# Optimization experiments

Measured on AMD Instinct MI355X. Metric: run time of the kernel, lower is better.

The kernel has to match this reference:

```python
import jax, jax.numpy as jnp
import numpy as np

B, T, EMB = 2, 2048, 1024
H, D = 16, 64          # n_heads, head_dim; H*D == EMB
FF = 4 * EMB


def _ln(x, w, b, eps=1e-5):
    mu = jnp.mean(x, axis=-1, keepdims=True)
    var = jnp.var(x, axis=-1, keepdims=True)
    return (x - mu) * jax.lax.rsqrt(var + eps) * w + b


def setup_inputs() -> dict:
    key = jax.random.key(0)
    ks = jax.random.split(key, 5)
    s = 0.02
    return {
        "x": jax.random.normal(ks[0], (B, T, EMB), jnp.float32),
        "ln1_w": jnp.ones((EMB,), jnp.float32),
        "ln1_b": jnp.zeros((EMB,), jnp.float32),
        "c_proj_w": jax.random.normal(ks[1], (3 * H * D, EMB), jnp.float32) * s,  # Linear(emb, 3HD, bias=False)
        "proj_w": jax.random.normal(ks[2], (EMB, H * D), jnp.float32) * s,
        "proj_b": jnp.zeros((EMB,), jnp.float32),
        "ln2_w": jnp.ones((EMB,), jnp.float32),
        "ln2_b": jnp.zeros((EMB,), jnp.float32),
        "ffn1_w": jax.random.normal(ks[3], (FF, EMB), jnp.float32) * s,
        "ffn1_b": jnp.zeros((FF,), jnp.float32),
        "ffn2_w": jax.random.normal(ks[4], (EMB, FF), jnp.float32) * s,
        "ffn2_b": jnp.zeros((EMB,), jnp.float32),
    }


def reference(x, ln1_w, ln1_b, c_proj_w, proj_w, proj_b, ln2_w, ln2_b,
              ffn1_w, ffn1_b, ffn2_w, ffn2_b):
    Bx, Tx, C = x.shape
    ln_x = _ln(x, ln1_w, ln1_b)
    c = ln_x @ c_proj_w.T                     # (B,T,3HD)
    c = c.reshape(Bx, Tx, H, 3 * D)
    k, q, v = jnp.split(c, 3, axis=-1)        # split order k,q,v as in source
    q = q.transpose(0, 2, 1, 3)               # (B,H,T,D)
    k = k.transpose(0, 2, 1, 3)
    v = v.transpose(0, 2, 1, 3)
    wei = jnp.einsum('bhqd,bhkd->bhqk', q, k) * (D ** -0.5)  # (B,H,T,T)
    mask = jnp.tril(jnp.ones((Tx, Tx), bool))
    wei = jnp.where(mask, wei, -jnp.inf)
    wei = jax.nn.softmax(wei, axis=-1)
    act = jnp.einsum('bhqk,bhkd->bhqd', wei, v)
    act = act.transpose(0, 2, 1, 3).reshape(Bx, Tx, H * D)
    act = act @ proj_w.T + proj_b
    act = x + act                              # residual 1
    h = _ln(act, ln2_w, ln2_b)
    h = jax.nn.relu(h @ ffn1_w.T + ffn1_b) @ ffn2_w.T + ffn2_b
    return x + h                               # NOTE: source adds x, not act
```

## Files before the change

kernel.cpp:

```cpp
#include <hip/hip_runtime.h>
#include <math.h>

typedef unsigned short u16;
typedef unsigned int u32;
typedef __attribute__((ext_vector_type(8))) __bf16 bf16x8;
typedef __attribute__((ext_vector_type(4))) float f32x4;

#define DEVI __device__ __forceinline__

DEVI u16 f2bf(float f){
  u32 b = __builtin_bit_cast(u32, f);
  return (u16)((b + 0x7FFFu + ((b >> 16) & 1u)) >> 16);
}

DEVI f32x4 mfma16(bf16x8 a, bf16x8 b, f32x4 c){
  return __builtin_amdgcn_mfma_f32_16x16x32_bf16(a, b, c, 0, 0, 0);
}

DEVI void gload16(const u16* g, u16* l){
  __builtin_amdgcn_global_load_lds(
      (const __attribute__((address_space(1))) u32*)g,
      (__attribute__((address_space(3))) u32*)l,
      16, 0, 0);
}

DEVI void phase_bar(){
  __builtin_amdgcn_sched_barrier(0);
  __builtin_amdgcn_s_barrier();
  __builtin_amdgcn_sched_barrier(0);
}

__global__ __launch_bounds__(256) void cvt_kernel(const float* __restrict__ in,
                                                  u16* __restrict__ out, int n4){
  int i = blockIdx.x * 256 + threadIdx.x;
  if (i >= n4) return;
  float4 v = reinterpret_cast<const float4*>(in)[i];
  u32 lo = (u32)f2bf(v.x) | ((u32)f2bf(v.y) << 16);
  u32 hi = (u32)f2bf(v.z) | ((u32)f2bf(v.w) << 16);
  reinterpret_cast<uint2*>(out)[i] = make_uint2(lo, hi);
}

__global__ __launch_bounds__(256) void ln_kernel(const float* __restrict__ x,
                                                 const float* __restrict__ w,
                                                 const float* __restrict__ b,
                                                 u16* __restrict__ out){
  int row = blockIdx.x;
  int tid = threadIdx.x;
  const float4 v = reinterpret_cast<const float4*>(x + (size_t)row * 1024)[tid];
  float s  = v.x + v.y + v.z + v.w;
  float ss = v.x*v.x + v.y*v.y + v.z*v.z + v.w*v.w;
  #pragma unroll
  for (int m = 1; m < 64; m <<= 1){
    s  += __shfl_xor(s,  m, 64);
    ss += __shfl_xor(ss, m, 64);
  }
  __shared__ float red[8];
  int wid = tid >> 6, lane = tid & 63;
  if (lane == 0){ red[wid] = s; red[4 + wid] = ss; }
  __syncthreads();
  s  = red[0] + red[1] + red[2] + red[3];
  ss = red[4] + red[5] + red[6] + red[7];
  float mu   = s * (1.0f/1024.0f);
  float var  = ss * (1.0f/1024.0f) - mu*mu;
  float rstd = rsqrtf(var + 1e-5f);
  const float4 wv = reinterpret_cast<const float4*>(w)[tid];
  const float4 bv = reinterpret_cast<const float4*>(b)[tid];
  u32 lo = (u32)f2bf((v.x-mu)*rstd*wv.x + bv.x) | ((u32)f2bf((v.y-mu)*rstd*wv.y + bv.y) << 16);
  u32 hi = (u32)f2bf((v.z-mu)*rstd*wv.z + bv.z) | ((u32)f2bf((v.w-mu)*rstd*wv.w + bv.w) << 16);
  reinterpret_cast<uint2*>(out + (size_t)row*1024)[tid] = make_uint2(lo, hi);
}

__global__ __launch_bounds__(256) void reduce4_kernel(const u16* __restrict__ P,
                                                      const float* __restrict__ x,
                                                      const float* __restrict__ bias,
                                                      float* __restrict__ out){
  const size_t i8 = ((size_t)blockIdx.x * 256 + threadIdx.x) * 8;
  const size_t PS = (size_t)4096 * 1024;
  const int col0 = (int)(i8 & 1023);
  float acc[8];
  #pragma unroll
  for (int j = 0; j < 8; ++j) acc[j] = bias[col0 + j];
  #pragma unroll
  for (int s = 0; s < 4; ++s){
    uint4 d = *reinterpret_cast<const uint4*>(P + s*PS + i8);
    u32 w[4] = {d.x, d.y, d.z, d.w};
    #pragma unroll
    for (int j = 0; j < 8; ++j){
      u32 bits = ((w[j>>1] >> (16*(j&1))) & 0xFFFFu) << 16;
      acc[j] += __builtin_bit_cast(float, bits);
    }
  }
  float4 xv0 = reinterpret_cast<const float4*>(x + i8)[0];
  float4 xv1 = reinterpret_cast<const float4*>(x + i8)[1];
  acc[0]+=xv0.x; acc[1]+=xv0.y; acc[2]+=xv0.z; acc[3]+=xv0.w;
  acc[4]+=xv1.x; acc[5]+=xv1.y; acc[6]+=xv1.z; acc[7]+=xv1.w;
  reinterpret_cast<float4*>(out + i8)[0] = make_float4(acc[0],acc[1],acc[2],acc[3]);
  reinterpret_cast<float4*>(out + i8)[1] = make_float4(acc[4],acc[5],acc[6],acc[7]);
}

template<bool HAS_BIAS, bool RELU, bool SPLIT>
__global__ __launch_bounds__(512, 2) void gemm256(const u16* __restrict__ A,
                                                  const u16* __restrict__ W,
                                                  const float* __restrict__ bias,
                                                  u16* __restrict__ outp,
                                                  int M, int N, int lda, int kLen){
  const int tid = threadIdx.x;
  const int wid = tid >> 6, lane = tid & 63;
  const int l16 = lane & 15, lhi = lane >> 4;
  const int wr = wid >> 2, wc = wid & 3;

  const int gx = gridDim.x, gy = gridDim.y;
  const int nwg = gx * gy * gridDim.z;
  const int bid = (blockIdx.z * gy + blockIdx.y) * gx + blockIdx.x;
  const int swz = (bid & 7) * (nwg >> 3) + (bid >> 3);
  const int col = swz % gx;
  const int rs  = swz / gx;
  const int row = rs % gy;
  const int ksp = rs / gy;
  const int brow = row * 256;
  const int bcol = col * 256;
  const size_t koff = (size_t)ksp * kLen;
  if (SPLIT) outp += (size_t)ksp * M * N;

  __shared__ u16 LDS[2][2][2][256*32];

  const int srow = tid >> 2;
  const int cg   = (tid & 3) ^ ((tid >> 3) & 3);
  const u16* gA = A + (size_t)(brow + srow) * lda + koff + cg*8;
  const u16* gW = W + (size_t)(bcol + srow) * lda + koff + cg*8;
  const size_t rK = (size_t)128 * lda;

#define STAGE(buf, mat, ks, t) do {                                   \
    const u16* _s = ((mat) ? gW : gA) + (t)*64 + (ks)*32;             \
    u16* _d = &LDS[buf][mat][ks][(wid*16)*32];                        \
    gload16(_s,      _d);                                             \
    gload16(_s + rK, _d + 128*32);                                    \
  } while(0)

  const int cswz = (lhi ^ ((l16 >> 1) & 3)) * 8;
  const int aoff = (wr*128 + l16)*32 + cswz;
  const int boff = (wc*64  + l16)*32 + cswz;
#define RDA(buf, ks, m) (*reinterpret_cast<const bf16x8*>(&LDS[buf][0][ks][aoff + (m)*512]))
#define RDB(buf, ks, n) (*reinterpret_cast<const bf16x8*>(&LDS[buf][1][ks][boff + (n)*512]))

  f32x4 acc[8][4] = {};
  bf16x8 a[8], b0, b1;

#define MFMA_PH(n0, n1) do {                                          \
    __builtin_amdgcn_s_setprio(1);                                    \
    _Pragma("unroll")                                                 \
    for (int m = 0; m < 8; ++m){                                      \
      acc[m][n0] = mfma16(a[m], b0, acc[m][n0]);                      \
      acc[m][n1] = mfma16(a[m], b1, acc[m][n1]);                      \
    }                                                                 \
    __builtin_amdgcn_s_setprio(0);                                    \
  } while(0)

  const int NITER = kLen >> 7;

  STAGE(0,0,0,0); STAGE(0,1,0,0); STAGE(0,0,1,0); STAGE(0,1,1,0);
  STAGE(1,0,0,1); STAGE(1,1,0,1);
  asm volatile("s_waitcnt vmcnt(4)" ::: "memory");
  phase_bar();

  for (int j = 0; j < NITER; ++j){
    const int t0 = 2*j, t1 = 2*j + 1;
    const bool more = (j + 1 < NITER);

    #pragma unroll
    for (int m = 0; m < 8; ++m) a[m] = RDA(0,0,m);
    b0 = RDB(0,0,0); b1 = RDB(0,0,1);
    STAGE(1,0,1,t1);
    phase_bar();
    MFMA_PH(0,1);
    phase_bar();
    b0 = RDB(0,0,2); b1 = RDB(0,0,3);
    STAGE(1,1,1,t1);
    phase_bar();
    MFMA_PH(2,3);
    phase_bar();
    #pragma unroll
    for (int m = 0; m < 8; ++m) a[m] = RDA(0,1,m);
    b0 = RDB(0,1,0); b1 = RDB(0,1,1);
    if (more) STAGE(0,0,0,t0+2);
    phase_bar();
    MFMA_PH(0,1);
    phase_bar();
    b0 = RDB(0,1,2); b1 = RDB(0,1,3);
    if (more){ STAGE(0,1,0,t0+2); asm volatile("s_waitcnt vmcnt(4)" ::: "memory"); }
    else     {                    asm volatile("s_waitcnt vmcnt(0)" ::: "memory"); }
    phase_bar();
    MFMA_PH(2,3);
    phase_bar();
    #pragma unroll
    for (int m = 0; m < 8; ++m) a[m] = RDA(1,0,m);
    b0 = RDB(1,0,0); b1 = RDB(1,0,1);
    if (more) STAGE(0,0,1,t0+2);
    phase_bar();
    MFMA_PH(0,1);
    phase_bar();
    b0 = RDB(1,0,2); b1 = RDB(1,0,3);
    if (more) STAGE(0,1,1,t0+2);
    phase_bar();
    MFMA_PH(2,3);
    phase_bar();
    #pragma unroll
    for (int m = 0; m < 8; ++m) a[m] = RDA(1,1,m);
    b0 = RDB(1,1,0); b1 = RDB(1,1,1);
    if (more) STAGE(1,0,0,t1+2);
    phase_bar();
    MFMA_PH(0,1);
    phase_bar();
    b0 = RDB(1,1,2); b1 = RDB(1,1,3);
    if (more){ STAGE(1,1,0,t1+2); asm volatile("s_waitcnt vmcnt(4)" ::: "memory"); }
    phase_bar();
    MFMA_PH(2,3);
    phase_bar();
  }
  __builtin_amdgcn_sched_barrier(0);

  const int row0 = brow + wr*128;
  const int col0 = bcol + wc*64;
  #pragma unroll
  for (int m = 0; m < 8; ++m){
    #pragma unroll
    for (int n = 0; n < 4; ++n){
      #pragma unroll
      for (int r = 0; r < 4; ++r){
        int row_ = row0 + m*16 + 4*lhi + r;
        int col_ = col0 + n*16 + l16;
        float v = acc[m][n][r];
        if constexpr (HAS_BIAS) v += bias[col_];
        if constexpr (RELU)     v = fmaxf(v, 0.0f);
        outp[(size_t)row_ * N + col_] = f2bf(v);
      }
    }
  }
#undef STAGE
#undef RDA
#undef RDB
#undef MFMA_PH
}

template<bool HAS_BIAS, bool HAS_RES, bool RELU, bool OUT_BF16>
__global__ __launch_bounds__(256) void gemm_bt(const u16* __restrict__ A,
                                               const u16* __restrict__ W,
                                               const float* __restrict__ bias,
                                               const float* __restrict__ res,
                                               void* __restrict__ outp,
                                               int M, int N, int K){
  const int tid = threadIdx.x;
  const int wid = tid >> 6, lane = tid & 63;
  const int l16 = lane & 15, lhi = lane >> 4;
  const int wr = wid >> 1, wc = wid & 1;

  const int gx = gridDim.x;
  const int nwg = gx * gridDim.y;
  const int bid = blockIdx.y * gx + blockIdx.x;
  const int swz = (bid & 7) * (nwg >> 3) + (bid >> 3);
  const int brow = (swz / gx) * 128;
  const int bcol = (swz % gx) * 128;

  __shared__ u16 As[2][128*32];
  __shared__ u16 Bs[2][128*32];

  const int srow = wid*32 + (lane >> 2);
  const int schk = lane & 3;
  const u16* gA0 = A + (size_t)(brow + srow)      * K + schk*8;
  const u16* gA1 = A + (size_t)(brow + srow + 16) * K + schk*8;
  const u16* gW0 = W + (size_t)(bcol + srow)      * K + schk*8;
  const u16* gW1 = W + (size_t)(bcol + srow + 16) * K + schk*8;
  const int ldsA0 = (wid*32)*32, ldsA1 = (wid*32 + 16)*32;

  f32x4 acc[4][4] = {};

  gload16(gA0, &As[0][ldsA0]);
  gload16(gA1, &As[0][ldsA1]);
  gload16(gW0, &Bs[0][ldsA0]);
  gload16(gW1, &Bs[0][ldsA1]);

  int cur = 0;
  for (int k0 = 0; k0 < K; k0 += 32){
    __syncthreads();
    if (k0 + 32 < K){
      gload16(gA0 + k0 + 32, &As[cur^1][ldsA0]);
      gload16(gA1 + k0 + 32, &As[cur^1][ldsA1]);
      gload16(gW0 + k0 + 32, &Bs[cur^1][ldsA0]);
      gload16(gW1 + k0 + 32, &Bs[cur^1][ldsA1]);
    }
    bf16x8 af[4], bfr[4];
    #pragma unroll
    for (int m = 0; m < 4; ++m)
      af[m]  = *reinterpret_cast<const bf16x8*>(&As[cur][(wr*64 + m*16 + l16)*32 + 8*lhi]);
    #pragma unroll
    for (int n = 0; n < 4; ++n)
      bfr[n] = *reinterpret_cast<const bf16x8*>(&Bs[cur][(wc*64 + n*16 + l16)*32 + 8*lhi]);
    #pragma unroll
    for (int m = 0; m < 4; ++m){
      #pragma unroll
      for (int n = 0; n < 4; ++n){
        acc[m][n] = mfma16(af[m], bfr[n], acc[m][n]);
      }
    }
    cur ^= 1;
  }

  const int row0 = brow + wr*64;
  const int col0 = bcol + wc*64;
  #pragma unroll
  for (int m = 0; m < 4; ++m){
    #pragma unroll
    for (int n = 0; n < 4; ++n){
      #pragma unroll
      for (int r = 0; r < 4; ++r){
        int row = row0 + m*16 + 4*lhi + r;
        int col = col0 + n*16 + l16;
        float v = acc[m][n][r];
        if constexpr (HAS_BIAS) v += bias[col];
        if constexpr (RELU)     v = fmaxf(v, 0.0f);
        if constexpr (HAS_RES)  v += res[(size_t)row * N + col];
        if constexpr (OUT_BF16) ((u16*)outp)[(size_t)row * N + col] = f2bf(v);
        else                    ((float*)outp)[(size_t)row * N + col] = v;
      }
    }
  }
}

__global__ __launch_bounds__(256) void attn_kernel(const u16* __restrict__ qkv,
                                                   u16* __restrict__ att){
  const int bh = blockIdx.x;
  const int qt = 31 - blockIdx.y;
  const int bb = bh >> 4, hh = bh & 15;
  const int tid = threadIdx.x;
  const int wid = tid >> 6, lane = tid & 63;
  const int l16 = lane & 15, lhi = lane >> 4;
  const u16* base = qkv + (size_t)bb * 2048 * 3072 + (size_t)hh * 192;

  __shared__ u16 Ks[64*72];
  __shared__ u16 Vt[64*72];
  __shared__ u16 Ps[4*16*72];

  const int sr = tid >> 2;
  const int sc = tid & 3;
  const u16* stage_base = base + (size_t)sr * 3072 + sc*8;

  const int qrow0 = qt * 64 + wid * 16;

  bf16x8 qf[2];
  {
    const u16* qp = base + (size_t)(qrow0 + l16) * 3072 + 64 + 8*lhi;
    qf[0] = *reinterpret_cast<const bf16x8*>(qp);
    qf[1] = *reinterpret_cast<const bf16x8*>(qp + 32);
  }

  f32x4 o[4] = {};
  float m_r[4], l_r[4];
  #pragma unroll
  for (int r = 0; r < 4; ++r){ m_r[r] = -INFINITY; l_r[r] = 0.0f; }

  const int nkt = qt + 1;

  uint4 kd0, kd1, vd0, vd1;
  {
    const u16* srow = stage_base;
    kd0 = *reinterpret_cast<const uint4*>(srow);
    kd1 = *reinterpret_cast<const uint4*>(srow + 32);
    vd0 = *reinterpret_cast<const uint4*>(srow + 128);
    vd1 = *reinterpret_cast<const uint4*>(srow + 160);
  }

  for (int kt = 0; kt < nkt; ++kt){
    __syncthreads();
    *reinterpret_cast<uint4*>(&Ks[sr*72 + sc*8])      = kd0;
    *reinterpret_cast<uint4*>(&Ks[sr*72 + sc*8 + 32]) = kd1;
    {
      u32 w0[4] = {vd0.x, vd0.y, vd0.z, vd0.w};
      u32 w1[4] = {vd1.x, vd1.y, vd1.z, vd1.w};
      const int ch0 = ((sr>>3) ^ sc)       << 3;
      const int ch1 = ((sr>>3) ^ (sc + 4)) << 3;
      #pragma unroll
      for (int j = 0; j < 8; ++j){
        int d0 = sc*8 + j;
        Vt[d0*72        + ch0 + (sr&7)] = (u16)(w0[j>>1] >> (16*(j&1)));
        Vt[(d0+32)*72   + ch1 + (sr&7)] = (u16)(w1[j>>1] >> (16*(j&1)));
      }
    }
    __syncthreads();

    if (kt + 1 < nkt){
      const u16* srow = stage_base + (size_t)(kt + 1) * 64 * 3072;
      kd0 = *reinterpret_cast<const uint4*>(srow);
      kd1 = *reinterpret_cast<const uint4*>(srow + 32);
      vd0 = *reinterpret_cast<const uint4*>(srow + 128);
      vd1 = *reinterpret_cast<const uint4*>(srow + 160);
    }

    const int kb = kt * 64;

    f32x4 s_acc[4] = {};
    #pragma unroll
    for (int f = 0; f < 4; ++f){
      const u16* kp = &Ks[(f*16 + l16)*72 + 8*lhi];
      bf16x8 k0 = *reinterpret_cast<const bf16x8*>(kp);
      bf16x8 k1 = *reinterpret_cast<const bf16x8*>(kp + 32);
      s_acc[f] = mfma16(qf[0], k0, s_acc[f]);
      s_acc[f] = mfma16(qf[1], k1, s_acc[f]);
    }

    float sc_[4][4];
    #pragma unroll
    for (int f = 0; f < 4; ++f){
      #pragma unroll
      for (int r = 0; r < 4; ++r) sc_[f][r] = s_acc[f][r] * 0.125f;
    }

    if (kt == nkt - 1){
      #pragma unroll
      for (int f = 0; f < 4; ++f){
        int col = kb + f*16 + l16;
        #pragma unroll
        for (int r = 0; r < 4; ++r){
          int row = qrow0 + 4*lhi + r;
          if (col > row) sc_[f][r] = -INFINITY;
        }
      }
    }

    float alpha[4], p[4][4];
    #pragma unroll
    for (int r = 0; r < 4; ++r){
      float mx = fmaxf(fmaxf(sc_[0][r], sc_[1][r]), fmaxf(sc_[2][r], sc_[3][r]));
      #pragma unroll
      for (int m = 1; m < 16; m <<= 1) mx = fmaxf(mx, __shfl_xor(mx, m, 64));
      float mnew = fmaxf(m_r[r], mx);
      alpha[r] = __expf(m_r[r] - mnew);
      m_r[r] = mnew;
      float sum = 0.0f;
      #pragma unroll
      for (int f = 0; f < 4; ++f){ p[f][r] = __expf(sc_[f][r] - mnew); sum += p[f][r]; }
      #pragma unroll
      for (int m = 1; m < 16; m <<= 1) sum += __shfl_xor(sum, m, 64);
      l_r[r] = l_r[r] * alpha[r] + sum;
    }
    #pragma unroll
    for (int n = 0; n < 4; ++n){
      #pragma unroll
      for (int r = 0; r < 4; ++r) o[n][r] *= alpha[r];
    }

    #pragma unroll
    for (int f = 0; f < 4; ++f){
      #pragma unroll
      for (int r = 0; r < 4; ++r)
        Ps[wid*1152 + (4*lhi + r)*72 + f*16 + l16] = f2bf(p[f][r]);
    }
    bf16x8 pa[2];
    pa[0] = *reinterpret_cast<const bf16x8*>(&Ps[wid*1152 + l16*72 + 8*lhi]);
    pa[1] = *reinterpret_cast<const bf16x8*>(&Ps[wid*1152 + l16*72 + 8*lhi + 32]);

    #pragma unroll
    for (int n = 0; n < 4; ++n){
      const int dv = n*16 + l16;
      const int dh = dv >> 3;
      #pragma unroll
      for (int s = 0; s < 2; ++s){
        const int ch = ((lhi + 4*s) ^ dh) << 3;
        bf16x8 vb = *reinterpret_cast<const bf16x8*>(&Vt[dv*72 + ch]);
        o[n] = mfma16(pa[s], vb, o[n]);
      }
    }
  }

  float inv_l[4];
  #pragma unroll
  for (int r = 0; r < 4; ++r) inv_l[r] = 1.0f / l_r[r];
  #pragma unroll
  for (int n = 0; n < 4; ++n){
    #pragma unroll
    for (int r = 0; r < 4; ++r){
      int row = qrow0 + 4*lhi + r;
      int col = hh*64 + n*16 + l16;
      att[(size_t)(bb*2048 + row) * 1024 + col] = f2bf(o[n][r] * inv_l[r]);
    }
  }
}

extern "C" void kernel_launch(void* const* d_in, const int* in_sizes, int n_in,
                              void* d_out, int out_size, void* d_ws, size_t ws_size,
                              hipStream_t stream){
  const float* x        = (const float*)d_in[0];
  const float* ln1_w    = (const float*)d_in[1];
  const float* ln1_b    = (const float*)d_in[2];
  const float* c_proj_w = (const float*)d_in[3];
  const float* proj_w   = (const float*)d_in[4];
  const float* proj_b   = (const float*)d_in[5];
  const float* ln2_w    = (const float*)d_in[6];
  const float* ln2_b    = (const float*)d_in[7];
  const float* ffn1_w   = (const float*)d_in[8];
  const float* ffn1_b   = (const float*)d_in[9];
  const float* ffn2_w   = (const float*)d_in[10];
  const float* ffn2_b   = (const float*)d_in[11];

  char* p = (char*)d_ws;
  u16* Wff1  = (u16*)p;  p += (size_t)4096*1024*2;
  u16* Wff2  = (u16*)p;  p += (size_t)1024*4096*2;
  u16* QKV   = (u16*)p;  p += (size_t)4096*3072*2;
  u16* ATT   = (u16*)p;  p += (size_t)4096*1024*2;
  u16* Wqkv  = (u16*)p;  p += (size_t)3072*1024*2;
  u16* Wproj = (u16*)p;  p += (size_t)1024*1024*2;
  u16* LNb   = (u16*)p;  p += (size_t)4096*1024*2;
  float* ACT2= (float*)p;
  u16* FFN1  = QKV;
  u16* PART  = Wqkv;

  cvt_kernel<<<3072, 256, 0, stream>>>(c_proj_w, Wqkv, 786432);
  cvt_kernel<<<1024, 256, 0, stream>>>(proj_w,  Wproj, 262144);
  cvt_kernel<<<4096, 256, 0, stream>>>(ffn1_w,  Wff1, 1048576);
  cvt_kernel<<<4096, 256, 0, stream>>>(ffn2_w,  Wff2, 1048576);

  ln_kernel<<<4096, 256, 0, stream>>>(x, ln1_w, ln1_b, LNb);
  gemm256<false,false,false><<<dim3(12,16,1), 512, 0, stream>>>(LNb, Wqkv, nullptr, QKV, 4096, 3072, 1024, 1024);
  attn_kernel<<<dim3(32,32), 256, 0, stream>>>(QKV, ATT);
  gemm_bt<true ,true ,false,false><<<dim3(8,32), 256, 0, stream>>>(ATT, Wproj, proj_b, x, ACT2, 4096, 1024, 1024);
  ln_kernel<<<4096, 256, 0, stream>>>(ACT2, ln2_w, ln2_b, LNb);
  gemm256<true ,true ,false><<<dim3(16,16,1), 512, 0, stream>>>(LNb, Wff1, ffn1_b, FFN1, 4096, 4096, 1024, 1024);
  gemm256<false,false,true ><<<dim3(4,16,4), 512, 0, stream>>>(FFN1, Wff2, nullptr, PART, 4096, 1024, 4096, 1024);
  reduce4_kernel<<<2048, 256, 0, stream>>>(PART, x, ffn2_b, (float*)d_out);
}
```

Baseline: 253.8 us.

## Rework attention softmax with exp2, lazy rescale, deferred row sums and swizzled LDS

Folds the softmax scale and log2(e) into Q once, so the inner loop can use exp2 without a per-score multiply. The running max is rescaled only when some lane sees a new maximum, and the row-sum reduction across lanes is moved to after the loop. The V transpose into LDS now writes packed 32-bit pairs into a padded, XOR-swizzled layout, the P buffer is swizzled the same way, and the MFMA sections get raised wave priority. Rounding the scaled Q to bf16 adds a small precision change, and the padding enlarges LDS use slightly.

```diff
diff --git a/kernel.cpp b/kernel.cpp
--- a/kernel.cpp
+++ b/kernel.cpp
@@ -28,6 +28,19 @@
   __builtin_amdgcn_sched_barrier(0);
   __builtin_amdgcn_s_barrier();
   __builtin_amdgcn_sched_barrier(0);
+}
+
+DEVI bf16x8 scale_bf16x8(bf16x8 v, float s){
+  u32 w[4]; __builtin_memcpy(w, &v, 16);
+  u32 o[4];
+  #pragma unroll
+  for (int i = 0; i < 4; ++i){
+    float f0 = __builtin_bit_cast(float, (w[i] & 0xFFFFu) << 16) * s;
+    float f1 = __builtin_bit_cast(float, w[i] & 0xFFFF0000u) * s;
+    o[i] = (u32)f2bf(f0) | ((u32)f2bf(f1) << 16);
+  }
+  bf16x8 r; __builtin_memcpy(&r, o, 16);
+  return r;
 }
 
 __global__ __launch_bounds__(256) void cvt_kernel(const float* __restrict__ in,
@@ -337,37 +350,39 @@
   const u16* base = qkv + (size_t)bb * 2048 * 3072 + (size_t)hh * 192;
 
   __shared__ u16 Ks[64*72];
-  __shared__ u16 Vt[64*72];
-  __shared__ u16 Ps[4*16*72];
+  __shared__ u16 Vt[64*80];
+  __shared__ u16 Ps[4*16*80];
 
   const int sr = tid >> 2;
   const int sc = tid & 3;
-  const u16* stage_base = base + (size_t)sr * 3072 + sc*8;
+  const u16* kstage = base + (size_t)sr * 3072 + sc*8;
+  const int va = tid >> 3;
+  const int vb = tid & 7;
+  const u16* vstage = base + (size_t)(2*va) * 3072 + 128 + vb*8;
+  const int vch = ((va >> 2) ^ vb) * 8 + 2*(va & 3);
 
   const int qrow0 = qt * 64 + wid * 16;
 
+  const float QSCALE = 0.125f * 1.44269504f;
   bf16x8 qf[2];
   {
     const u16* qp = base + (size_t)(qrow0 + l16) * 3072 + 64 + 8*lhi;
-    qf[0] = *reinterpret_cast<const bf16x8*>(qp);
-    qf[1] = *reinterpret_cast<const bf16x8*>(qp + 32);
+    qf[0] = scale_bf16x8(*reinterpret_cast<const bf16x8*>(qp), QSCALE);
+    qf[1] = scale_bf16x8(*reinterpret_cast<const bf16x8*>(qp + 32), QSCALE);
   }
 
   f32x4 o[4] = {};
-  float m_r[4], l_r[4];
-  #pragma unroll
-  for (int r = 0; r < 4; ++r){ m_r[r] = -INFINITY; l_r[r] = 0.0f; }
+  float m_r[4], l_part[4];
+  #pragma unroll
+  for (int r = 0; r < 4; ++r){ m_r[r] = -INFINITY; l_part[r] = 0.0f; }
 
   const int nkt = qt + 1;
 
   uint4 kd0, kd1, vd0, vd1;
-  {
-    const u16* srow = stage_base;
-    kd0 = *reinterpret_cast<const uint4*>(srow);
-    kd1 = *reinterpret_cast<const uint4*>(srow + 32);
-    vd0 = *reinterpret_cast<const uint4*>(srow + 128);
-    vd1 = *reinterpret_cast<const uint4*>(srow + 160);
-  }
+  kd0 = *reinterpret_cast<const uint4*>(kstage);
+  kd1 = *reinterpret_cast<const uint4*>(kstage + 32);
+  vd0 = *reinterpret_cast<const uint4*>(vstage);
+  vd1 = *reinterpret_cast<const uint4*>(vstage + 3072);
 
   for (int kt = 0; kt < nkt; ++kt){
     __syncthreads();
@@ -376,28 +391,29 @@
     {
       u32 w0[4] = {vd0.x, vd0.y, vd0.z, vd0.w};
       u32 w1[4] = {vd1.x, vd1.y, vd1.z, vd1.w};
-      const int ch0 = ((sr>>3) ^ sc)       << 3;
-      const int ch1 = ((sr>>3) ^ (sc + 4)) << 3;
-      #pragma unroll
-      for (int j = 0; j < 8; ++j){
-        int d0 = sc*8 + j;
-        Vt[d0*72        + ch0 + (sr&7)] = (u16)(w0[j>>1] >> (16*(j&1)));
-        Vt[(d0+32)*72   + ch1 + (sr&7)] = (u16)(w1[j>>1] >> (16*(j&1)));
+      #pragma unroll
+      for (int jj = 0; jj < 8; ++jj){
+        u32 e0 = (w0[jj>>1] >> (16*(jj&1))) & 0xFFFFu;
+        u32 e1 = (w1[jj>>1] >> (16*(jj&1))) & 0xFFFFu;
+        int d = vb*8 + jj;
+        *reinterpret_cast<u32*>(&Vt[d*80 + vch]) = e0 | (e1 << 16);
       }
     }
     __syncthreads();
 
     if (kt + 1 < nkt){
-      const u16* srow = stage_base + (size_t)(kt + 1) * 64 * 3072;
-      kd0 = *reinterpret_cast<const uint4*>(srow);
-      kd1 = *reinterpret_cast<const uint4*>(srow + 32);
-      vd0 = *reinterpret_cast<const uint4*>(srow + 128);
-      vd1 = *reinterpret_cast<const uint4*>(srow + 160);
+      const u16* kp = kstage + (size_t)(kt + 1) * 64 * 3072;
+      const u16* vp = vstage + (size_t)(kt + 1) * 64 * 3072;
+      kd0 = *reinterpret_cast<const uint4*>(kp);
+      kd1 = *reinterpret_cast<const uint4*>(kp + 32);
+      vd0 = *reinterpret_cast<const uint4*>(vp);
+      vd1 = *reinterpret_cast<const uint4*>(vp + 3072);
     }
 
     const int kb = kt * 64;
 
     f32x4 s_acc[4] = {};
+    __builtin_amdgcn_s_setprio(1);
     #pragma unroll
     for (int f = 0; f < 4; ++f){
       const u16* kp = &Ks[(f*16 + l16)*72 + 8*lhi];
@@ -406,12 +422,13 @@
       s_acc[f] = mfma16(qf[0], k0, s_acc[f]);
       s_acc[f] = mfma16(qf[1], k1, s_acc[f]);
     }
+    __builtin_amdgcn_s_setprio(0);
 
     float sc_[4][4];
     #pragma unroll
     for (int f = 0; f < 4; ++f){
       #pragma unroll
-      for (int r = 0; r < 4; ++r) sc_[f][r] = s_acc[f][r] * 0.125f;
+      for (int r = 0; r < 4; ++r) sc_[f][r] = s_acc[f][r];
     }
 
     if (kt == nkt - 1){
@@ -426,54 +443,71 @@
       }
     }
 
-    float alpha[4], p[4][4];
+    float mxl[4];
+    bool need = false;
     #pragma unroll
     for (int r = 0; r < 4; ++r){
-      float mx = fmaxf(fmaxf(sc_[0][r], sc_[1][r]), fmaxf(sc_[2][r], sc_[3][r]));
-      #pragma unroll
-      for (int m = 1; m < 16; m <<= 1) mx = fmaxf(mx, __shfl_xor(mx, m, 64));
-      float mnew = fmaxf(m_r[r], mx);
-      alpha[r] = __expf(m_r[r] - mnew);
-      m_r[r] = mnew;
-      float sum = 0.0f;
-      #pragma unroll
-      for (int f = 0; f < 4; ++f){ p[f][r] = __expf(sc_[f][r] - mnew); sum += p[f][r]; }
-      #pragma unroll
-      for (int m = 1; m < 16; m <<= 1) sum += __shfl_xor(sum, m, 64);
-      l_r[r] = l_r[r] * alpha[r] + sum;
-    }
+      mxl[r] = fmaxf(fmaxf(sc_[0][r], sc_[1][r]), fmaxf(sc_[2][r], sc_[3][r]));
+      need |= (mxl[r] > m_r[r]);
+    }
+    if (__any(need)){
+      #pragma unroll
+      for (int r = 0; r < 4; ++r){
+        float mx = mxl[r];
+        #pragma unroll
+        for (int m = 1; m < 16; m <<= 1) mx = fmaxf(mx, __shfl_xor(mx, m, 64));
+        float mnew = fmaxf(m_r[r], mx);
+        float al = exp2f(m_r[r] - mnew);
+        m_r[r] = mnew;
+        l_part[r] *= al;
+        #pragma unroll
+        for (int n = 0; n < 4; ++n) o[n][r] *= al;
+      }
+    }
+    float p[4][4];
+    #pragma unroll
+    for (int r = 0; r < 4; ++r){
+      float s0 = 0.0f;
+      #pragma unroll
+      for (int f = 0; f < 4; ++f){ p[f][r] = exp2f(sc_[f][r] - m_r[r]); s0 += p[f][r]; }
+      l_part[r] += s0;
+    }
+
+    #pragma unroll
+    for (int f = 0; f < 4; ++f){
+      const int kk = f*16 + l16;
+      #pragma unroll
+      for (int r = 0; r < 4; ++r){
+        const int q = 4*lhi + r;
+        Ps[wid*1280 + q*80 + (((kk>>3) ^ (q&7))*8) + (kk&7)] = f2bf(p[f][r]);
+      }
+    }
+    bf16x8 pa[2];
+    pa[0] = *reinterpret_cast<const bf16x8*>(&Ps[wid*1280 + l16*80 + (((lhi    ) ^ (l16&7))*8)]);
+    pa[1] = *reinterpret_cast<const bf16x8*>(&Ps[wid*1280 + l16*80 + (((lhi + 4) ^ (l16&7))*8)]);
+
+    __builtin_amdgcn_s_setprio(1);
     #pragma unroll
     for (int n = 0; n < 4; ++n){
-      #pragma unroll
-      for (int r = 0; r < 4; ++r) o[n][r] *= alpha[r];
-    }
-
-    #pragma unroll
-    for (int f = 0; f < 4; ++f){
-      #pragma unroll
-      for (int r = 0; r < 4; ++r)
-        Ps[wid*1152 + (4*lhi + r)*72 + f*16 + l16] = f2bf(p[f][r]);
-    }
-    bf16x8 pa[2];
-    pa[0] = *reinterpret_cast<const bf16x8*>(&Ps[wid*1152 + l16*72 + 8*lhi]);
-    pa[1] = *reinterpret_cast<const bf16x8*>(&Ps[wid*1152 + l16*72 + 8*lhi + 32]);
-
-    #pragma unroll
-    for (int n = 0; n < 4; ++n){
-      const int dv = n*16 + l16;
-      const int dh = dv >> 3;
+      const int d = n*16 + l16;
+      const int dh = d >> 3;
       #pragma unroll
       for (int s = 0; s < 2; ++s){
-        const int ch = ((lhi + 4*s) ^ dh) << 3;
-        bf16x8 vb = *reinterpret_cast<const bf16x8*>(&Vt[dv*72 + ch]);
-        o[n] = mfma16(pa[s], vb, o[n]);
-      }
-    }
+        bf16x8 vfr = *reinterpret_cast<const bf16x8*>(&Vt[d*80 + (((lhi + 4*s) ^ dh)*8)]);
+        o[n] = mfma16(pa[s], vfr, o[n]);
+      }
+    }
+    __builtin_amdgcn_s_setprio(0);
   }
 
   float inv_l[4];
   #pragma unroll
-  for (int r = 0; r < 4; ++r) inv_l[r] = 1.0f / l_r[r];
+  for (int r = 0; r < 4; ++r){
+    float l = l_part[r];
+    #pragma unroll
+    for (int m = 1; m < 16; m <<= 1) l += __shfl_xor(l, m, 64);
+    inv_l[r] = 1.0f / l;
+  }
   #pragma unroll
   for (int n = 0; n < 4; ++n){
     #pragma unroll
```

Result: no change. 249.2 us (-1.8%).
